# Optimization experiments

Hardware: AMD Instinct MI355X
Metric: run time of the kernel (lower is better)

Reference implementation:

```python
import jax, jax.numpy as jnp
import numpy as np

B, S, C, NH = 4, 2048, 1024, 16
HD = C // NH


def setup_inputs() -> dict:
    key = jax.random.key(0)
    ks = jax.random.split(key, 8)
    w = lambda k, shape: (jax.random.normal(k, shape, dtype=jnp.float32) * 0.02)
    return {
        "x": jax.random.normal(ks[0], (B, S, C), dtype=jnp.float32),
        "y": jax.random.normal(ks[1], (B, S, C), dtype=jnp.float32),
        "mask": jnp.zeros((B, S), dtype=bool),  # True = padded key
        "Wq_w": w(ks[2], (C, C)),
        "Wq_b": jnp.zeros((C,), dtype=jnp.float32),
        "Wkv_w": w(ks[3], (2 * C, C)),
        "Wkv_b": jnp.zeros((2 * C,), dtype=jnp.float32),
        "Wo_w": w(ks[4], (C, C)),
        "Wo_b": jnp.zeros((C,), dtype=jnp.float32),
    }


def reference(x, y, mask, Wq_w, Wq_b, Wkv_w, Wkv_b, Wo_w, Wo_b):
    b, s, c = x.shape
    # projections (torch nn.Linear: x @ W.T + b)
    q = (x @ Wq_w.T + Wq_b).reshape(b, s, NH, HD).transpose(0, 2, 1, 3)  # bhsd
    kv = (y @ Wkv_w.T + Wkv_b).reshape(b, s, 2, NH, HD)
    k = kv[:, :, 0].transpose(0, 2, 1, 3)  # bhsd
    v = kv[:, :, 1].transpose(0, 2, 1, 3)  # bhsd
    # scores: [b, h, s_q, s_k]
    attn = jnp.einsum("bhqd,bhkd->bhqk", q, k) / np.sqrt(HD).astype(np.float32)
    causal = jnp.triu(jnp.ones((s, s), dtype=bool), 1)  # True above diagonal
    combined = causal[None, None] | mask[:, None, None, :]
    attn = jnp.where(combined, -jnp.inf, attn)
    attn = jax.nn.softmax(attn, axis=-1)
    out = jnp.einsum("bhqk,bhkd->bhqd", attn, v)
    out = out.transpose(0, 2, 1, 3).reshape(b, s, c)
    return out @ Wo_w.T + Wo_b
```

## Files before the change

### kernel.cpp

```cpp
#include <hip/hip_runtime.h>
#include <stdint.h>

#define B_  4
#define S_  2048
#define C_  1024
#define NH_ 16
#define HD_ 64
#define M_  (B_*S_)
#define NT_ (S_/64)
#define NKT 16

typedef __attribute__((ext_vector_type(8))) short bf16x8;
typedef __attribute__((ext_vector_type(4))) float f32x4;

typedef __attribute__((address_space(1))) const unsigned int gu32;
typedef __attribute__((address_space(3))) unsigned int lu32;

__device__ __forceinline__ void gload16(const void* g, void* l) {
    __builtin_amdgcn_global_load_lds((gu32*)g, (lu32*)l, 16, 0, 0);
}

__device__ __forceinline__ unsigned short f2bf(float f) {
    union { float f; unsigned u; } v; v.f = f;
    unsigned r = v.u + 0x7FFF + ((v.u >> 16) & 1);
    return (unsigned short)(r >> 16);
}

__global__ __launch_bounds__(256)
void cvt_all(const float4* __restrict__ x, const float4* __restrict__ y,
             const float4* __restrict__ wq, const float4* __restrict__ wkv,
             const float4* __restrict__ wo,
             uint4* __restrict__ xb, uint4* __restrict__ yb, uint4* __restrict__ wqb,
             uint4* __restrict__ wkvb, uint4* __restrict__ wob) {
    int i = blockIdx.x * 256 + threadIdx.x;
    const float4* src; uint4* dst; int off;
    if      (i < 1048576) { src = x;   dst = xb;   off = i; }
    else if (i < 2097152) { src = y;   dst = yb;   off = i - 1048576; }
    else if (i < 2228224) { src = wq;  dst = wqb;  off = i - 2097152; }
    else if (i < 2490368) { src = wkv; dst = wkvb; off = i - 2228224; }
    else                  { src = wo;  dst = wob;  off = i - 2490368; }
    float4 a = src[2*off], b = src[2*off+1];
    union { unsigned short s[8]; uint4 v; } u;
    u.s[0]=f2bf(a.x); u.s[1]=f2bf(a.y); u.s[2]=f2bf(a.z); u.s[3]=f2bf(a.w);
    u.s[4]=f2bf(b.x); u.s[5]=f2bf(b.y); u.s[6]=f2bf(b.z); u.s[7]=f2bf(b.w);
    dst[off] = u.v;
}


#define STAGE_U(u, kb, db) \
    gload16(gA + (size_t)(u)*64*1024 + (kb), sh + (db)*24576 + ((u)*64 + w*8)*64)
#define STAGE_V(v, kb, db) \
    gload16(gB + (size_t)(v)*64*1024 + (kb), sh + (db)*24576 + 16384 + ((v)*64 + w*8)*64)
#define STAGE_ALL(kb, db) do { \
    STAGE_U(0, kb, db); STAGE_U(1, kb, db); STAGE_U(2, kb, db); STAGE_U(3, kb, db); \
    STAGE_V(0, kb, db); STAGE_V(1, kb, db); \
} while (0)

#define READ_AB(h) do { \
    const int co = colb ^ ((h)*32); \
    _Pragma("unroll") \
    for (int mf = 0; mf < 4; ++mf) \
        af[mf] = *(const bf16x8*)&Asb[(wq*64 + mf*16 + l16)*64 + co]; \
    _Pragma("unroll") \
    for (int nf = 0; nf < 4; ++nf) \
        bfr[nf] = *(const bf16x8*)&Bsb[(wx*64 + nf*16 + l16)*64 + co]; \
} while (0)

#define MFMA16() do { \
    _Pragma("unroll") \
    for (int mf = 0; mf < 4; ++mf) \
        _Pragma("unroll") \
        for (int nf = 0; nf < 4; ++nf) \
            acc[mf][nf] = __builtin_amdgcn_mfma_f32_16x16x32_bf16(af[mf], bfr[nf], acc[mf][nf], 0, 0, 0); \
} while (0)

template<int MODE>
__device__ __forceinline__
void gemm256_body(const unsigned short* __restrict__ A, const unsigned short* __restrict__ Bt,
                  const float* __restrict__ bias,
                  unsigned short* __restrict__ out0, unsigned short* __restrict__ out1,
                  float* __restrict__ outf, int bx, int by, unsigned short* sh)
{
    const int t = threadIdx.x;
    const int lane = t & 63, w = t >> 6;
    const int quad = lane >> 4, l16 = lane & 15;
    const int wq = w >> 1, wx = w & 1;
    const int s7 = l16 & 7;
    const int colb = (quad ^ s7) << 3;
    const int c16 = (lane & 7) ^ (lane >> 3);

    const int rowA0 = by * 256;
    const int colB0 = bx * 128;

    const unsigned short* gA = A  + (size_t)(rowA0 + w*8 + (lane>>3))*1024 + c16*8;
    const unsigned short* gB = Bt + (size_t)(colB0 + w*8 + (lane>>3))*1024 + c16*8;

    f32x4 acc[4][4] = {};
    bf16x8 af[4], bfr[4];

    STAGE_ALL(0, 0);
    STAGE_ALL(64, 1);
    asm volatile("s_waitcnt vmcnt(6)" ::: "memory");
    __builtin_amdgcn_s_barrier();
    __builtin_amdgcn_sched_barrier(0);

    #pragma unroll 1
    for (int kt = 0; kt < NKT; ++kt) {
        const int cur = kt & 1;
        const unsigned short* Asb = sh + cur*24576;
        const unsigned short* Bsb = Asb + 16384;
        const int kb2 = (kt + 2) * 64;
        const bool st2 = (kt + 2 < NKT);

        READ_AB(0);
        __builtin_amdgcn_s_setprio(1);
        MFMA16();
        __builtin_amdgcn_s_setprio(0);

        READ_AB(1);
        if (st2) {
            asm volatile("s_waitcnt lgkmcnt(0)" ::: "memory");
            __builtin_amdgcn_sched_barrier(0);
            __builtin_amdgcn_s_barrier();
            STAGE_ALL(kb2, cur);
        }
        __builtin_amdgcn_s_setprio(1);
        MFMA16();
        __builtin_amdgcn_s_setprio(0);

        if      (st2)           asm volatile("s_waitcnt vmcnt(6)" ::: "memory");
        else if (kt == NKT - 2) asm volatile("s_waitcnt vmcnt(0)" ::: "memory");
        if (kt < NKT - 1) {
            __builtin_amdgcn_s_barrier();
            __builtin_amdgcn_sched_barrier(0);
        }
    }

    const float QSCALE = 0.180336880111f;
    #pragma unroll
    for (int nf = 0; nf < 4; ++nf) {
        int gn = colB0 + wx*64 + nf*16 + l16;
        float bv = bias[gn];
        #pragma unroll
        for (int mf = 0; mf < 4; ++mf) {
            #pragma unroll
            for (int r = 0; r < 4; ++r) {
                int gm = rowA0 + wq*64 + mf*16 + quad*4 + r;
                float v = acc[mf][nf][r] + bv;
                if (MODE == 2) {
                    outf[(size_t)gm * 1024 + gn] = v;
                } else if (MODE == 0) {
                    v *= QSCALE;
                    int b = gm >> 11, s = gm & 2047;
                    int h = gn >> 6,  d = gn & 63;
                    out0[(((size_t)(b*NH_ + h)*S_ + s) << 6) + d] = f2bf(v);
                } else {
                    int b = gm >> 11, s = gm & 2047;
                    if (gn < C_) {
                        int h = gn >> 6, d = gn & 63;
                        out0[(((size_t)(b*NH_ + h)*S_ + s) << 6) + d] = f2bf(v);
                    } else {
                        int n2 = gn - C_;
                        int h = n2 >> 6, d = n2 & 63;
                        out1[((size_t)(b*NH_ + h)*HD_ + d)*S_ + s] = f2bf(v);
                    }
                }
            }
        }
    }
}

__global__ __launch_bounds__(512, 2)
void proj_fused256(const unsigned short* __restrict__ xb, const unsigned short* __restrict__ Wqb,
                   const float* __restrict__ Wq_b,
                   const unsigned short* __restrict__ yb, const unsigned short* __restrict__ Wkvb,
                   const float* __restrict__ Wkv_b,
                   unsigned short* __restrict__ Qg, unsigned short* __restrict__ Kg,
                   unsigned short* __restrict__ Vt)
{
    extern __shared__ unsigned short sh[];
    int bid = blockIdx.x;
    int id = (bid & 7) * 96 + (bid >> 3);
    if (id < 256) {
        gemm256_body<0>(xb, Wqb, Wq_b, Qg, nullptr, nullptr, id & 7, id >> 3, sh);
    } else {
        int j = id - 256;
        gemm256_body<1>(yb, Wkvb, Wkv_b, Kg, Vt, nullptr, j & 15, j >> 4, sh);
    }
}

__global__ __launch_bounds__(512, 2)
void gemm_oproj256(const unsigned short* __restrict__ A, const unsigned short* __restrict__ Bt,
                   const float* __restrict__ bias, float* __restrict__ outf)
{
    extern __shared__ unsigned short sh[];
    int id = ((blockIdx.x & 7) << 5) + (blockIdx.x >> 3);
    gemm256_body<2>(A, Bt, bias, nullptr, nullptr, outf, id & 7, id >> 3, sh);
}

__global__ __launch_bounds__(256, 4)
void attn_kernel(const unsigned short* __restrict__ Qg, const unsigned short* __restrict__ Kg,
                 const unsigned short* __restrict__ Vt, const unsigned char* __restrict__ maskp,
                 unsigned short* __restrict__ att)
{
    __shared__ unsigned short Pl[64*72];
    __shared__ float Lbuf[4][64];
    __shared__ float Linv[64];
    int t = threadIdx.x, lane = t & 63, w = t >> 6;
    int quad = lane >> 4, l16 = lane & 15;
    int bh = blockIdx.x, b = bh >> 4, h = bh & 15;
    int qi = blockIdx.y;

    const unsigned short* kbase = Kg + ((size_t)bh*S_ + w*16 + l16)*HD_ + quad*8;
    const unsigned short* vbase = Vt + ((size_t)bh*HD_ + w*16 + l16)*S_ + quad*8;
    int kp_row = w*16 + quad*4;
    const unsigned char* mbase = maskp + (size_t)b*S_ + kp_row;

    for (int half = 0; half < 2; ++half) {
        int qt = half ? (NT_ - 1 - qi) : qi;

        bf16x8 qf[4][2];
        #pragma unroll
        for (int m = 0; m < 4; ++m) {
            const unsigned short* qp = Qg + ((size_t)bh*S_ + qt*64 + m*16 + l16)*HD_;
            qf[m][0] = *reinterpret_cast<const bf16x8*>(qp + quad*8);
            qf[m][1] = *reinterpret_cast<const bf16x8*>(qp + 32 + quad*8);
        }
        f32x4 oacc[4] = {};
        float lsum[4] = {0.f, 0.f, 0.f, 0.f};

        bf16x8 kc0 = *reinterpret_cast<const bf16x8*>(kbase);
        bf16x8 kc1 = *reinterpret_cast<const bf16x8*>(kbase + 32);

        for (int kt = 0; kt <= qt; ++kt) {
            int ktn = (kt < qt) ? kt + 1 : kt;
            const unsigned short* kpn = kbase + (size_t)ktn*64*HD_;
            bf16x8 kn0 = *reinterpret_cast<const bf16x8*>(kpn);
            bf16x8 kn1 = *reinterpret_cast<const bf16x8*>(kpn + 32);
            const unsigned short* vp = vbase + kt*64;
            bf16x8 vc0 = *reinterpret_cast<const bf16x8*>(vp);
            bf16x8 vc1 = *reinterpret_cast<const bf16x8*>(vp + 32);

            unsigned m4 = *reinterpret_cast<const unsigned*>(mbase + kt*64);

            f32x4 sacc[4];
            #pragma unroll
            for (int m = 0; m < 4; ++m) {
                sacc[m] = __builtin_amdgcn_mfma_f32_16x16x32_bf16(kc0, qf[m][0], f32x4{}, 0, 0, 0);
                sacc[m] = __builtin_amdgcn_mfma_f32_16x16x32_bf16(kc1, qf[m][1], sacc[m], 0, 0, 0);
            }

            bool diag = (kt == qt);
            #pragma unroll
            for (int m = 0; m < 4; ++m) {
                float p[4];
                if (diag) {
                    #pragma unroll
                    for (int r = 0; r < 4; ++r) {
                        float s = sacc[m][r];
                        if (kp_row + r > m*16 + l16) s = -1e30f;
                        p[r] = __builtin_amdgcn_exp2f(s);
                    }
                } else {
                    #pragma unroll
                    for (int r = 0; r < 4; ++r)
                        p[r] = __builtin_amdgcn_exp2f(sacc[m][r]);
                }
                if (m4) {
                    #pragma unroll
                    for (int r = 0; r < 4; ++r)
                        if ((m4 >> (8*r)) & 0xFFu) p[r] = 0.f;
                }
                lsum[m] += (p[0] + p[1]) + (p[2] + p[3]);
                unsigned a01 = __builtin_amdgcn_perm(__float_as_uint(p[1]), __float_as_uint(p[0]), 0x07060302u);
                unsigned a23 = __builtin_amdgcn_perm(__float_as_uint(p[3]), __float_as_uint(p[2]), 0x07060302u);
                *reinterpret_cast<uint2*>(&Pl[(m*16 + l16)*72 + w*16 + quad*4]) = make_uint2(a01, a23);
            }
            __syncthreads();
            #pragma unroll
            for (int m = 0; m < 4; ++m) {
                bf16x8 pf0 = *reinterpret_cast<const bf16x8*>(&Pl[(m*16 + l16)*72 + quad*8]);
                bf16x8 pf1 = *reinterpret_cast<const bf16x8*>(&Pl[(m*16 + l16)*72 + 32 + quad*8]);
                oacc[m] = __builtin_amdgcn_mfma_f32_16x16x32_bf16(pf0, vc0, oacc[m], 0, 0, 0);
                oacc[m] = __builtin_amdgcn_mfma_f32_16x16x32_bf16(pf1, vc1, oacc[m], 0, 0, 0);
            }
            __syncthreads();
            kc0 = kn0; kc1 = kn1;
        }

        #pragma unroll
        for (int m = 0; m < 4; ++m) {
            lsum[m] += __shfl_xor(lsum[m], 16, 64);
            lsum[m] += __shfl_xor(lsum[m], 32, 64);
            Lbuf[w][m*16 + l16] = lsum[m];
        }
        __syncthreads();
        int q64 = t & 63;
        Linv[q64] = 1.0f / (Lbuf[0][q64] + Lbuf[1][q64] + Lbuf[2][q64] + Lbuf[3][q64]);
        __syncthreads();
        #pragma unroll
        for (int m = 0; m < 4; ++m) {
            #pragma unroll
            for (int r = 0; r < 4; ++r) {
                float iv = Linv[m*16 + quad*4 + r];
                int q = qt*64 + m*16 + quad*4 + r;
                att[((size_t)(b*S_ + q))*C_ + h*HD_ + w*16 + l16] = f2bf(oacc[m][r] * iv);
            }
        }
        __syncthreads();
    }
}

extern "C" void kernel_launch(void* const* d_in, const int* in_sizes, int n_in,
                              void* d_out, int out_size, void* d_ws, size_t ws_size,
                              hipStream_t stream) {
    const float* x     = (const float*)d_in[0];
    const float* y     = (const float*)d_in[1];
    const unsigned char* mask = (const unsigned char*)d_in[2];
    const float* Wq_w  = (const float*)d_in[3];
    const float* Wq_b  = (const float*)d_in[4];
    const float* Wkv_w = (const float*)d_in[5];
    const float* Wkv_b = (const float*)d_in[6];
    const float* Wo_w  = (const float*)d_in[7];
    const float* Wo_b  = (const float*)d_in[8];
    float* out = (float*)d_out;

    unsigned short* xb   = (unsigned short*)d_ws;
    unsigned short* yb   = xb   + (size_t)M_*C_;
    unsigned short* Wqb  = yb   + (size_t)M_*C_;
    unsigned short* Wkvb = Wqb  + (size_t)C_*C_;
    unsigned short* Wob  = Wkvb + (size_t)2*C_*C_;
    unsigned short* Qg   = Wob  + (size_t)C_*C_;
    unsigned short* Kg   = Qg   + (size_t)M_*C_;
    unsigned short* Vtg  = Kg   + (size_t)M_*C_;
    unsigned short* att  = xb;

    static bool once = []() {
        hipFuncSetAttribute((const void*)proj_fused256, hipFuncAttributeMaxDynamicSharedMemorySize, 98304);
        hipFuncSetAttribute((const void*)gemm_oproj256, hipFuncAttributeMaxDynamicSharedMemorySize, 98304);
        return true;
    }();
    (void)once;

    cvt_all<<<10240, 256, 0, stream>>>((const float4*)x, (const float4*)y,
        (const float4*)Wq_w, (const float4*)Wkv_w, (const float4*)Wo_w,
        (uint4*)xb, (uint4*)yb, (uint4*)Wqb, (uint4*)Wkvb, (uint4*)Wob);

    proj_fused256<<<768, 512, 98304, stream>>>(xb, Wqb, Wq_b, yb, Wkvb, Wkv_b, Qg, Kg, Vtg);
    attn_kernel<<<dim3(B_*NH_, NT_/2), 256, 0, stream>>>(Qg, Kg, Vtg, mask, att);
    gemm_oproj256<<<256, 512, 98304, stream>>>(att, Wob, Wo_b, out);
}
```

Baseline: 308.7 us.

## Shrink GEMM tiles to 128x128 single-buffered and add setprio in attention

Replaces the 256x128 double-buffered, 512-thread projection GEMMs (98 KB dynamic LDS, custom waitcnt and barrier pipeline) with 128x128 tiles on 256 threads, using 32 KB of static LDS and a simple load-sync-compute loop. The grid grows to 1536 and 512 blocks, aiming for more blocks per CU and better wave balance. The cost is losing the prefetch overlap, since each k-step now waits on its own global loads, plus more redundant global reads from the smaller tiles. The attention kernel also raises wave priority around its MFMA sections.

Measured after the change: 305.0 us. About the same (-1.2%).

```diff
diff --git a/kernel.cpp b/kernel.cpp
--- a/kernel.cpp
+++ b/kernel.cpp
@@ -47,23 +47,21 @@
 }
 
 
-#define STAGE_U(u, kb, db) \
-    gload16(gA + (size_t)(u)*64*1024 + (kb), sh + (db)*24576 + ((u)*64 + w*8)*64)
-#define STAGE_V(v, kb, db) \
-    gload16(gB + (size_t)(v)*64*1024 + (kb), sh + (db)*24576 + 16384 + ((v)*64 + w*8)*64)
-#define STAGE_ALL(kb, db) do { \
-    STAGE_U(0, kb, db); STAGE_U(1, kb, db); STAGE_U(2, kb, db); STAGE_U(3, kb, db); \
-    STAGE_V(0, kb, db); STAGE_V(1, kb, db); \
+#define STAGE_A(u, kb) gload16(gA + (size_t)(u)*8*1024 + (kb), shA + (w*32 + (u)*8)*64)
+#define STAGE_B(u, kb) gload16(gB + (size_t)(u)*8*1024 + (kb), shB + (w*32 + (u)*8)*64)
+#define STAGE_ALL(kb) do { \
+    STAGE_A(0, kb); STAGE_A(1, kb); STAGE_A(2, kb); STAGE_A(3, kb); \
+    STAGE_B(0, kb); STAGE_B(1, kb); STAGE_B(2, kb); STAGE_B(3, kb); \
 } while (0)
 
 #define READ_AB(h) do { \
     const int co = colb ^ ((h)*32); \
     _Pragma("unroll") \
     for (int mf = 0; mf < 4; ++mf) \
-        af[mf] = *(const bf16x8*)&Asb[(wq*64 + mf*16 + l16)*64 + co]; \
+        af[mf] = *(const bf16x8*)&shA[(wy*64 + mf*16 + l16)*64 + co]; \
     _Pragma("unroll") \
     for (int nf = 0; nf < 4; ++nf) \
-        bfr[nf] = *(const bf16x8*)&Bsb[(wx*64 + nf*16 + l16)*64 + co]; \
+        bf[nf] = *(const bf16x8*)&shB[(wx*64 + nf*16 + l16)*64 + co]; \
 } while (0)
 
 #define MFMA16() do { \
@@ -71,69 +69,45 @@
     for (int mf = 0; mf < 4; ++mf) \
         _Pragma("unroll") \
         for (int nf = 0; nf < 4; ++nf) \
-            acc[mf][nf] = __builtin_amdgcn_mfma_f32_16x16x32_bf16(af[mf], bfr[nf], acc[mf][nf], 0, 0, 0); \
+            acc[mf][nf] = __builtin_amdgcn_mfma_f32_16x16x32_bf16(af[mf], bf[nf], acc[mf][nf], 0, 0, 0); \
 } while (0)
 
 template<int MODE>
 __device__ __forceinline__
-void gemm256_body(const unsigned short* __restrict__ A, const unsigned short* __restrict__ Bt,
+void gemm128_body(const unsigned short* __restrict__ A, const unsigned short* __restrict__ Bt,
                   const float* __restrict__ bias,
                   unsigned short* __restrict__ out0, unsigned short* __restrict__ out1,
-                  float* __restrict__ outf, int bx, int by, unsigned short* sh)
+                  float* __restrict__ outf, int bx, int by,
+                  unsigned short* shA, unsigned short* shB)
 {
     const int t = threadIdx.x;
     const int lane = t & 63, w = t >> 6;
     const int quad = lane >> 4, l16 = lane & 15;
-    const int wq = w >> 1, wx = w & 1;
-    const int s7 = l16 & 7;
-    const int colb = (quad ^ s7) << 3;
+    const int wy = w >> 1, wx = w & 1;
+    const int colb = (quad ^ (l16 & 7)) << 3;
     const int c16 = (lane & 7) ^ (lane >> 3);
 
-    const int rowA0 = by * 256;
+    const int rowA0 = by * 128;
     const int colB0 = bx * 128;
 
-    const unsigned short* gA = A  + (size_t)(rowA0 + w*8 + (lane>>3))*1024 + c16*8;
-    const unsigned short* gB = Bt + (size_t)(colB0 + w*8 + (lane>>3))*1024 + c16*8;
+    const unsigned short* gA = A  + (size_t)(rowA0 + w*32 + (lane>>3))*1024 + c16*8;
+    const unsigned short* gB = Bt + (size_t)(colB0 + w*32 + (lane>>3))*1024 + c16*8;
 
     f32x4 acc[4][4] = {};
-    bf16x8 af[4], bfr[4];
-
-    STAGE_ALL(0, 0);
-    STAGE_ALL(64, 1);
-    asm volatile("s_waitcnt vmcnt(6)" ::: "memory");
-    __builtin_amdgcn_s_barrier();
-    __builtin_amdgcn_sched_barrier(0);
+    bf16x8 af[4], bf[4];
+
+    STAGE_ALL(0);
+    __syncthreads();
 
     #pragma unroll 1
     for (int kt = 0; kt < NKT; ++kt) {
-        const int cur = kt & 1;
-        const unsigned short* Asb = sh + cur*24576;
-        const unsigned short* Bsb = Asb + 16384;
-        const int kb2 = (kt + 2) * 64;
-        const bool st2 = (kt + 2 < NKT);
-
         READ_AB(0);
-        __builtin_amdgcn_s_setprio(1);
         MFMA16();
-        __builtin_amdgcn_s_setprio(0);
-
         READ_AB(1);
-        if (st2) {
-            asm volatile("s_waitcnt lgkmcnt(0)" ::: "memory");
-            __builtin_amdgcn_sched_barrier(0);
-            __builtin_amdgcn_s_barrier();
-            STAGE_ALL(kb2, cur);
-        }
-        __builtin_amdgcn_s_setprio(1);
         MFMA16();
-        __builtin_amdgcn_s_setprio(0);
-
-        if      (st2)           asm volatile("s_waitcnt vmcnt(6)" ::: "memory");
-        else if (kt == NKT - 2) asm volatile("s_waitcnt vmcnt(0)" ::: "memory");
-        if (kt < NKT - 1) {
-            __builtin_amdgcn_s_barrier();
-            __builtin_amdgcn_sched_barrier(0);
-        }
+        __syncthreads();
+        if (kt + 1 < NKT) STAGE_ALL((kt + 1) * 64);
+        __syncthreads();
     }
 
     const float QSCALE = 0.180336880111f;
@@ -145,7 +119,7 @@
         for (int mf = 0; mf < 4; ++mf) {
             #pragma unroll
             for (int r = 0; r < 4; ++r) {
-                int gm = rowA0 + wq*64 + mf*16 + quad*4 + r;
+                int gm = rowA0 + wy*64 + mf*16 + quad*4 + r;
                 float v = acc[mf][nf][r] + bv;
                 if (MODE == 2) {
                     outf[(size_t)gm * 1024 + gn] = v;
@@ -170,32 +144,34 @@
     }
 }
 
-__global__ __launch_bounds__(512, 2)
-void proj_fused256(const unsigned short* __restrict__ xb, const unsigned short* __restrict__ Wqb,
+__global__ __launch_bounds__(256, 3)
+void proj_fused128(const unsigned short* __restrict__ xb, const unsigned short* __restrict__ Wqb,
                    const float* __restrict__ Wq_b,
                    const unsigned short* __restrict__ yb, const unsigned short* __restrict__ Wkvb,
                    const float* __restrict__ Wkv_b,
                    unsigned short* __restrict__ Qg, unsigned short* __restrict__ Kg,
                    unsigned short* __restrict__ Vt)
 {
-    extern __shared__ unsigned short sh[];
+    __shared__ unsigned short shA[128*64];
+    __shared__ unsigned short shB[128*64];
     int bid = blockIdx.x;
-    int id = (bid & 7) * 96 + (bid >> 3);
-    if (id < 256) {
-        gemm256_body<0>(xb, Wqb, Wq_b, Qg, nullptr, nullptr, id & 7, id >> 3, sh);
+    int id = (bid & 7) * 192 + (bid >> 3);
+    if (id < 512) {
+        gemm128_body<0>(xb, Wqb, Wq_b, Qg, nullptr, nullptr, id & 7, id >> 3, shA, shB);
     } else {
-        int j = id - 256;
-        gemm256_body<1>(yb, Wkvb, Wkv_b, Kg, Vt, nullptr, j & 15, j >> 4, sh);
+        int j = id - 512;
+        gemm128_body<1>(yb, Wkvb, Wkv_b, Kg, Vt, nullptr, j & 15, j >> 4, shA, shB);
     }
 }
 
-__global__ __launch_bounds__(512, 2)
-void gemm_oproj256(const unsigned short* __restrict__ A, const unsigned short* __restrict__ Bt,
+__global__ __launch_bounds__(256, 3)
+void gemm_oproj128(const unsigned short* __restrict__ A, const unsigned short* __restrict__ Bt,
                    const float* __restrict__ bias, float* __restrict__ outf)
 {
-    extern __shared__ unsigned short sh[];
-    int id = ((blockIdx.x & 7) << 5) + (blockIdx.x >> 3);
-    gemm256_body<2>(A, Bt, bias, nullptr, nullptr, outf, id & 7, id >> 3, sh);
+    __shared__ unsigned short shA[128*64];
+    __shared__ unsigned short shB[128*64];
+    int id = ((blockIdx.x & 7) << 6) + (blockIdx.x >> 3);
+    gemm128_body<2>(A, Bt, bias, nullptr, nullptr, outf, id & 7, id >> 3, shA, shB);
 }
 
 __global__ __launch_bounds__(256, 4)
@@ -244,11 +220,13 @@
             unsigned m4 = *reinterpret_cast<const unsigned*>(mbase + kt*64);
 
             f32x4 sacc[4];
+            __builtin_amdgcn_s_setprio(1);
             #pragma unroll
             for (int m = 0; m < 4; ++m) {
                 sacc[m] = __builtin_amdgcn_mfma_f32_16x16x32_bf16(kc0, qf[m][0], f32x4{}, 0, 0, 0);
                 sacc[m] = __builtin_amdgcn_mfma_f32_16x16x32_bf16(kc1, qf[m][1], sacc[m], 0, 0, 0);
             }
+            __builtin_amdgcn_s_setprio(0);
 
             bool diag = (kt == qt);
             #pragma unroll
@@ -277,6 +255,7 @@
                 *reinterpret_cast<uint2*>(&Pl[(m*16 + l16)*72 + w*16 + quad*4]) = make_uint2(a01, a23);
             }
             __syncthreads();
+            __builtin_amdgcn_s_setprio(1);
             #pragma unroll
             for (int m = 0; m < 4; ++m) {
                 bf16x8 pf0 = *reinterpret_cast<const bf16x8*>(&Pl[(m*16 + l16)*72 + quad*8]);
@@ -284,6 +263,7 @@
                 oacc[m] = __builtin_amdgcn_mfma_f32_16x16x32_bf16(pf0, vc0, oacc[m], 0, 0, 0);
                 oacc[m] = __builtin_amdgcn_mfma_f32_16x16x32_bf16(pf1, vc1, oacc[m], 0, 0, 0);
             }
+            __builtin_amdgcn_s_setprio(0);
             __syncthreads();
             kc0 = kn0; kc1 = kn1;
         }
@@ -335,18 +315,11 @@
     unsigned short* Vtg  = Kg   + (size_t)M_*C_;
     unsigned short* att  = xb;
 
-    static bool once = []() {
-        hipFuncSetAttribute((const void*)proj_fused256, hipFuncAttributeMaxDynamicSharedMemorySize, 98304);
-        hipFuncSetAttribute((const void*)gemm_oproj256, hipFuncAttributeMaxDynamicSharedMemorySize, 98304);
-        return true;
-    }();
-    (void)once;
-
     cvt_all<<<10240, 256, 0, stream>>>((const float4*)x, (const float4*)y,
         (const float4*)Wq_w, (const float4*)Wkv_w, (const float4*)Wo_w,
         (uint4*)xb, (uint4*)yb, (uint4*)Wqb, (uint4*)Wkvb, (uint4*)Wob);
 
-    proj_fused256<<<768, 512, 98304, stream>>>(xb, Wqb, Wq_b, yb, Wkvb, Wkv_b, Qg, Kg, Vtg);
+    proj_fused128<<<1536, 256, 0, stream>>>(xb, Wqb, Wq_b, yb, Wkvb, Wkv_b, Qg, Kg, Vtg);
     attn_kernel<<<dim3(B_*NH_, NT_/2), 256, 0, stream>>>(Qg, Kg, Vtg, mask, att);
-    gemm_oproj256<<<256, 512, 98304, stream>>>(att, Wob, Wo_b, out);
-}
+    gemm_oproj128<<<512, 256, 0, stream>>>(att, Wob, Wo_b, out);
+}
```
